# Kernel tuning notes

Measured on AMD Instinct MI355X. Metric: run time of the kernel, lower is better.

The kernel has to match this reference:

```python
import jax, jax.numpy as jnp
import numpy as np

L, N, H, SQ = 24, 16384, 128, 32
D_OP, D_ATTR, D_FILT, D_OUT = 16, 56, 74, 32
D_IN = 2 * SQ + D_OP + D_ATTR  # 136
EPS = 1e-5
SLOPE = 0.01  # LeakyReLU default


def setup_inputs() -> dict:
    key = jax.random.key(0)
    ks = jax.random.split(key, 24)
    f32 = jnp.float32
    inp = {
        'op_pad': jax.random.normal(ks[0], (L, N, D_OP), f32),
        'attr_pad': jax.random.normal(ks[1], (L, N, D_ATTR), f32),
        'filter_pad': jax.random.normal(ks[2], (L, N, D_FILT), f32),
        'output_pad': jax.random.normal(ks[3], (L, N, D_OUT), f32),
        'mapping_pad': jax.random.randint(ks[4], (L, N, 2), 0, N + 1, jnp.int32),
        'batch_size': 4096,
        # filter / output squeeze linears
        'Wf': jax.random.normal(ks[5], (SQ, D_FILT), f32) * 0.05,
        'bf': jax.random.normal(ks[6], (SQ,), f32) * 0.05,
        'Wo': jax.random.normal(ks[7], (SQ, D_OUT), f32) * 0.05,
        'bo': jax.random.normal(ks[8], (SQ,), f32) * 0.05,
        # batchnorm affine params
        'g1': jnp.ones((SQ,), f32), 'beta1': jnp.zeros((SQ,), f32),
        'g2': jnp.ones((SQ,), f32), 'beta2': jnp.zeros((SQ,), f32),
        # LSTM (PyTorch layout: gates i,f,g,o stacked)
        'Wih': jax.random.normal(ks[9], (4 * H, D_IN), f32) * 0.05,
        'Whh': jax.random.normal(ks[10], (4 * H, H), f32) * 0.05,
        'bih': jax.random.normal(ks[11], (4 * H,), f32) * 0.05,
        'bhh': jax.random.normal(ks[12], (4 * H,), f32) * 0.05,
        # final MLP head
        'W1': jax.random.normal(ks[13], (20, H), f32) * 0.05,
        'b1': jax.random.normal(ks[14], (20,), f32) * 0.05,
        'W2': jax.random.normal(ks[15], (1, 20), f32) * 0.05,
        'b2': jax.random.normal(ks[16], (1,), f32) * 0.05,
    }
    return inp


def _leaky(x):
    return jnp.where(x > 0, x, SLOPE * x)


def _bn(x, g, b):
    # BatchNorm1d in training mode: batch stats (biased var), eps=1e-5
    m = jnp.mean(x, axis=0)
    v = jnp.var(x, axis=0)
    return (x - m) * jax.lax.rsqrt(v + EPS) * g + b


def _forward(op_pad, attr_pad, filter_pad, output_pad, mapping_pad, batch_size,
             Wf, bf, Wo, bo, g1, beta1, g2, beta2, Wih, Whh, bih, bhh, W1, b1, W2, b2):
    l, n = op_pad.shape[0], op_pad.shape[1]
    # squeeze filter / output features, flattened over (L*N)
    fd = _bn(_leaky(filter_pad.reshape(l * n, -1) @ Wf.T + bf), g1, beta1).reshape(l, n, SQ)
    od = _bn(_leaky(output_pad.reshape(l * n, -1) @ Wo.T + bo), g2, beta2).reshape(l, n, SQ)
    lstm_in = jnp.concatenate([op_pad, attr_pad, fd, od], axis=2)  # [L,N,D_IN]

    def step(carry, xs):
        h, c = carry                       # [N,H] previous level states
        x, mapping = xs                    # [N,D_IN], [N,2]
        mask = (mapping != 0)[..., None]   # [N,2,1]
        idx = jnp.maximum(mapping - 1, 0)  # [N,2] gather indices
        gh = jnp.sum(jnp.where(mask, h[idx], 0.0), axis=1) * 0.5  # [N,H]
        gc = jnp.sum(jnp.where(mask, c[idx], 0.0), axis=1) * 0.5
        gates = x @ Wih.T + bih + gh @ Whh.T + bhh  # [N,4H]
        i, f, g, o = jnp.split(gates, 4, axis=1)
        c_new = jax.nn.sigmoid(f) * gc + jax.nn.sigmoid(i) * jnp.tanh(g)
        h_new = jax.nn.sigmoid(o) * jnp.tanh(c_new)
        return (h_new, c_new), None

    z = jnp.zeros((n, H), lstm_in.dtype)
    # loop goes from the deepest level (index L-1) up to 0
    (h, _), _ = jax.lax.scan(step, (z, z), (lstm_in[::-1], mapping_pad[::-1]))
    out = h[:batch_size]
    out = jax.nn.sigmoid((out @ W1.T + b1) @ W2.T + b2)  # [B,1]
    return out


def reference(op_pad, attr_pad, filter_pad, output_pad, mapping_pad, batch_size,
              Wf, bf, Wo, bo, g1, beta1, g2, beta2, Wih, Whh, bih, bhh, W1, b1, W2, b2):
    return _forward(op_pad, attr_pad, filter_pad, output_pad, mapping_pad, batch_size,
                    Wf, bf, Wo, bo, g1, beta1, g2, beta2, Wih, Whh, bih, bhh, W1, b1, W2, b2)
```

## Files before the change

kernel.cpp:

```cpp
#include <hip/hip_runtime.h>
#include <hip/hip_bf16.h>

#define LL 24
#define NN 16384
#define HH 128
#define KP 288
#define LN (LL*NN)

typedef __bf16 bf16;
typedef __attribute__((ext_vector_type(8))) __bf16 bf16x8;
typedef __attribute__((ext_vector_type(4))) __bf16 bf16x4;
typedef __attribute__((ext_vector_type(2))) __bf16 bf16x2;
typedef __attribute__((ext_vector_type(4))) float f32x4;

__device__ __forceinline__ float sigm(float x){ return 1.f/(1.f+__expf(-x)); }
__device__ __forceinline__ float tanhfast(float x){
    float e = __expf(-2.f*fabsf(x));
    float t = (1.f-e)/(1.f+e);
    return x >= 0.f ? t : -t;
}
__device__ __forceinline__ void gld16(const void* g, void* l){
    __builtin_amdgcn_global_load_lds(
        (const __attribute__((address_space(1))) void*)g,
        (__attribute__((address_space(3))) void*)l, 16, 0, 0);
}

template<int D, int DP, int NQ, int TILES>
__global__ __launch_bounds__(256) void act_kernel(
    const float* __restrict__ X, const float* __restrict__ W,
    const float* __restrict__ bias, bf16* __restrict__ act,
    float* __restrict__ sums)
{
    __shared__ float xs[192*DP];
    const int tid = threadIdx.x;
    const int cg  = tid & 7;
    const int rg  = tid >> 3;
    const int rbase = rg*6;

    float bc[4];
    #pragma unroll
    for (int c=0;c<4;++c) bc[c] = bias[cg*4+c];

    float s[4] = {0,0,0,0}, qq[4] = {0,0,0,0};

    for (int tile = blockIdx.x; tile < TILES; tile += gridDim.x) {
        __syncthreads();
        const float* Xt = X + (size_t)tile * (192*D);
        for (int i = tid; i < 192*D; i += 256) {
            int r = i / D, c = i - r*D;
            xs[r*DP + c] = Xt[i];
        }
        if constexpr (4*NQ > D) {
            constexpr int PADW = 4*NQ - D;
            for (int i = tid; i < 192*PADW; i += 256) {
                int r = i / PADW, c = i - r*PADW;
                xs[r*DP + D + c] = 0.f;
            }
        }
        __syncthreads();

        float a[6][4];
        #pragma unroll
        for (int i=0;i<6;++i)
            #pragma unroll
            for (int c=0;c<4;++c) a[i][c] = 0.f;

        #pragma unroll 2
        for (int q = 0; q < NQ; ++q) {
            float4 wv[4];
            #pragma unroll
            for (int c = 0; c < 4; ++c) {
                const float* wp = W + (cg*4 + c)*D + q*4;
                if constexpr (D % 4 == 0) {
                    wv[c] = *(const float4*)wp;
                } else {
                    if ((4*NQ > D) && (q == NQ-1)) {
                        float2 lo = *(const float2*)wp;
                        wv[c] = make_float4(lo.x, lo.y, 0.f, 0.f);
                    } else {
                        float2 lo = *(const float2*)wp;
                        float2 hi = *(const float2*)(wp+2);
                        wv[c] = make_float4(lo.x, lo.y, hi.x, hi.y);
                    }
                }
            }
            #pragma unroll
            for (int i = 0; i < 6; ++i) {
                float4 xv = *(const float4*)&xs[(rbase+i)*DP + q*4];
                #pragma unroll
                for (int c = 0; c < 4; ++c) {
                    a[i][c] = fmaf(xv.x, wv[c].x, a[i][c]);
                    a[i][c] = fmaf(xv.y, wv[c].y, a[i][c]);
                    a[i][c] = fmaf(xv.z, wv[c].z, a[i][c]);
                    a[i][c] = fmaf(xv.w, wv[c].w, a[i][c]);
                }
            }
        }

        #pragma unroll
        for (int i = 0; i < 6; ++i) {
            bf16x4 pk;
            #pragma unroll
            for (int c = 0; c < 4; ++c) {
                float v = a[i][c] + bc[c];
                v = v > 0.f ? v : 0.01f*v;
                pk[c] = (bf16)v;
                s[c] += v; qq[c] += v*v;
            }
            *(bf16x4*)&act[((size_t)tile*192 + rbase + i)*32 + cg*4] = pk;
        }
    }

    __syncthreads();
    float* red = xs;
    #pragma unroll
    for (int c=0;c<4;++c){ red[tid*8 + c*2] = s[c]; red[tid*8 + c*2 + 1] = qq[c]; }
    __syncthreads();
    if (tid < 64) {
        const int ch = tid >> 1, v = tid & 1;
        const int cgr = ch >> 2, cl = ch & 3;
        float t = 0.f;
        for (int r = 0; r < 32; ++r)
            t += red[(r*8 + cgr)*8 + cl*2 + v];
        atomicAdd(&sums[v*32 + ch], t);
    }
}

__global__ void prep_wtb(const float* __restrict__ Wih, const float* __restrict__ Whh,
                         const float* __restrict__ bih, const float* __restrict__ bhh,
                         bf16* __restrict__ Wtb, float* __restrict__ b4p)
{
    const int np = blockIdx.x;
    const int k  = threadIdx.x;
    const int gate = (np>>4)&3;
    const int j = gate*128 + (np>>6)*16 + (np&15);
    if (k < KP) {
        float v = 0.f;
        if (k < 136)      v = Wih[(long)j*136 + k];
        else if (k >= 160) v = Whh[(long)j*128 + (k-160)];
        Wtb[(long)np*KP + k] = (bf16)v;
    }
    if (k == 0) b4p[np] = bih[j] + bhh[j];
}

__global__ void prep_stats(const float* __restrict__ stats,
    const float* __restrict__ g1, const float* __restrict__ beta1,
    const float* __restrict__ g2, const float* __restrict__ beta2,
    const float* __restrict__ W1, const float* __restrict__ b1,
    const float* __restrict__ W2, const float* __restrict__ b2,
    float* __restrict__ ss, float* __restrict__ wvb)
{
    const int t = threadIdx.x;
    const float inv = 1.f/(float)LN;
    if (t < 32) {
        float mean = stats[t]*inv;
        float var  = stats[32+t]*inv - mean*mean;
        float sc = g1[t]/sqrtf(var + 1e-5f);
        ss[t] = sc; ss[32+t] = beta1[t] - mean*sc;
    } else if (t < 64) {
        int c = t - 32;
        float mean = stats[64+c]*inv;
        float var  = stats[96+c]*inv - mean*mean;
        float sc = g2[c]/sqrtf(var + 1e-5f);
        ss[64+c] = sc; ss[96+c] = beta2[c] - mean*sc;
    }
    float s = 0.f;
    for (int a=0;a<20;++a) s += W2[a]*W1[a*HH + t];
    wvb[t] = s;
    if (t == 0) {
        float sb = 0.f;
        for (int a=0;a<20;++a) sb += W2[a]*b1[a];
        wvb[128] = sb + b2[0];
    }
}

__global__ __launch_bounds__(256) void build_a(
    const float* __restrict__ op, const float* __restrict__ attr,
    const bf16* __restrict__ actf, const bf16* __restrict__ acto,
    const int* __restrict__ map, const float* __restrict__ ss,
    const bf16* __restrict__ h_prev, bf16* __restrict__ A,
    int l, int first)
{
    const int n0 = blockIdx.x * 32;
    const long lbase = (long)l * NN;
    for (int i = threadIdx.x; i < 32*36; i += 256) {
        const int r = i / 36, c = i - r*36;
        const long n = n0 + r;
        const long e = lbase + n;
        const int k0 = c*8;
        bf16x8 out;
        if (c < 9) {
            const float* src = (c < 2) ? (op + e*16 + k0) : (attr + e*56 + (k0-16));
            float4 f0 = *(const float4*)src;
            float4 f1 = *(const float4*)(src+4);
            out[0]=(bf16)f0.x; out[1]=(bf16)f0.y; out[2]=(bf16)f0.z; out[3]=(bf16)f0.w;
            out[4]=(bf16)f1.x; out[5]=(bf16)f1.y; out[6]=(bf16)f1.z; out[7]=(bf16)f1.w;
        } else if (c < 17) {
            const int ch = (c < 13) ? (k0-72) : (k0-104);
            const bf16* src = (c < 13) ? (actf + e*32 + ch) : (acto + e*32 + ch);
            const float* s = ss + ((c < 13) ? 0 : 64);
            bf16x8 v = *(const bf16x8*)src;
            #pragma unroll
            for (int j=0;j<8;++j)
                out[j] = (bf16)fmaf((float)v[j], s[ch+j], s[32+ch+j]);
        } else if (c < 20) {
            #pragma unroll
            for (int j=0;j<8;++j) out[j] = (bf16)0.f;
        } else {
            const int jj = k0 - 160;
            float g[8] = {0,0,0,0,0,0,0,0};
            if (!first) {
                int2 mp = *(const int2*)&map[e*2];
                if (mp.x) { bf16x8 v = *(const bf16x8*)&h_prev[(long)(mp.x-1)*HH + jj];
                    #pragma unroll
                    for (int j=0;j<8;++j) g[j] += (float)v[j]; }
                if (mp.y) { bf16x8 v = *(const bf16x8*)&h_prev[(long)(mp.y-1)*HH + jj];
                    #pragma unroll
                    for (int j=0;j<8;++j) g[j] += (float)v[j]; }
            }
            #pragma unroll
            for (int j=0;j<8;++j) out[j] = (bf16)(0.5f*g[j]);
        }
        *(bf16x8*)&A[n*KP + k0] = out;
    }
}

__global__ __launch_bounds__(256) void lstm_gemm(
    const bf16* __restrict__ A, const bf16* __restrict__ Wtb,
    const float* __restrict__ b4p, const int* __restrict__ map,
    const float* __restrict__ c_prev, float* __restrict__ c_next,
    bf16* __restrict__ h_next, int l, int first)
{
    __shared__ bf16 As[128*32];
    __shared__ bf16 Bs[128*32];
    const int tid  = threadIdx.x;
    const int bm   = blockIdx.x;
    const int bn   = blockIdx.y;
    const int m0   = bm*128, n0p = bn*128;
    const int lane = tid & 63, w = tid >> 6;
    const int wr   = w >> 1,  wc = w & 1;

    f32x4 acc[4][4];
    #pragma unroll
    for (int ni=0; ni<4; ++ni){
        float b = b4p[n0p + wc*64 + ni*16 + (lane&15)];
        #pragma unroll
        for (int mi=0; mi<4; ++mi) acc[mi][ni] = (f32x4){b,b,b,b};
    }

    const bf16* Ab = A   + (size_t)m0*KP;
    const bf16* Bb = Wtb + (size_t)n0p*KP;
    const int lrr = lane >> 2;
    const int qs  = lane & 3;

    for (int kk=0; kk<9; ++kk){
        __syncthreads();
        #pragma unroll
        for (int hh=0; hh<2; ++hh){
            const int lr = w*32 + hh*16 + lrr;
            const int q  = qs ^ ((lr>>1)&3);
            const size_t go = (size_t)lr*KP + kk*32 + q*8;
            gld16(Ab + go, &As[(w*32 + hh*16)*32]);
            gld16(Bb + go, &Bs[(w*32 + hh*16)*32]);
        }
        __syncthreads();
        bf16x8 af[4], bfr[4];
        #pragma unroll
        for (int t4=0; t4<4; ++t4){
            const int am = wr*64 + t4*16 + (lane&15);
            af[t4] = *(const bf16x8*)&As[am*32 + (((lane>>4) ^ ((am>>1)&3))<<3)];
            const int bn_ = wc*64 + t4*16 + (lane&15);
            bfr[t4] = *(const bf16x8*)&Bs[bn_*32 + (((lane>>4) ^ ((bn_>>1)&3))<<3)];
        }
        #pragma unroll
        for (int mi=0; mi<4; ++mi)
            #pragma unroll
            for (int ni=0; ni<4; ++ni)
                acc[mi][ni] = __builtin_amdgcn_mfma_f32_16x16x32_bf16(
                    af[mi], bfr[ni], acc[mi][ni], 0, 0, 0);
    }

    const long lbase = (long)l * NN;
    const int cell = bn*32 + wc*16 + (lane&15);
    #pragma unroll
    for (int mi=0; mi<4; ++mi){
        const int rbase = m0 + wr*64 + mi*16 + (lane>>4)*4;
        #pragma unroll
        for (int reg=0; reg<4; ++reg){
            const int n = rbase + reg;
            float gc = 0.f;
            if (!first){
                int2 mp = *(const int2*)&map[(lbase+n)*2];
                if (mp.x) gc += c_prev[(long)(mp.x-1)*HH + cell];
                if (mp.y) gc += c_prev[(long)(mp.y-1)*HH + cell];
                gc *= 0.5f;
            }
            float cn = sigm(acc[mi][1][reg])*gc
                     + sigm(acc[mi][0][reg])*tanhfast(acc[mi][2][reg]);
            float hn = sigm(acc[mi][3][reg])*tanhfast(cn);
            c_next[(long)n*HH + cell] = cn;
            h_next[(long)n*HH + cell] = (bf16)hn;
        }
    }
}

__global__ __launch_bounds__(256) void final_k(
    const bf16* __restrict__ h, const float* __restrict__ wvb,
    float* __restrict__ out, int rows)
{
    int gt = blockIdx.x*256 + threadIdx.x;
    int row = gt >> 6;
    int lane = gt & 63;
    if (row >= rows) return;
    float v = fmaf((float)h[(long)row*HH + lane], wvb[lane],
                   (float)h[(long)row*HH + 64 + lane] * wvb[64+lane]);
    #pragma unroll
    for (int off=32; off>0; off>>=1) v += __shfl_down(v, off);
    if (lane == 0) out[row] = sigm(v + wvb[128]);
}

extern "C" void kernel_launch(void* const* d_in, const int* in_sizes, int n_in,
                              void* d_out, int out_size, void* d_ws, size_t ws_size,
                              hipStream_t stream)
{
    const float* op      = (const float*)d_in[0];
    const float* attr    = (const float*)d_in[1];
    const float* filt    = (const float*)d_in[2];
    const float* outp    = (const float*)d_in[3];
    const int*   mapping = (const int*)d_in[4];
    const float* Wf  = (const float*)d_in[6];
    const float* bf_ = (const float*)d_in[7];
    const float* Wo  = (const float*)d_in[8];
    const float* bo  = (const float*)d_in[9];
    const float* g1  = (const float*)d_in[10];
    const float* be1 = (const float*)d_in[11];
    const float* g2  = (const float*)d_in[12];
    const float* be2 = (const float*)d_in[13];
    const float* Wih = (const float*)d_in[14];
    const float* Whh = (const float*)d_in[15];
    const float* bih = (const float*)d_in[16];
    const float* bhh = (const float*)d_in[17];
    const float* W1  = (const float*)d_in[18];
    const float* b1  = (const float*)d_in[19];
    const float* W2  = (const float*)d_in[20];
    const float* b2  = (const float*)d_in[21];

    char* p = (char*)d_ws;
    auto alloc = [&](size_t bytes){ char* r = p; p += (bytes + 255) & ~255ull; return r; };
    bf16* actf = (bf16*)alloc((size_t)LN*32*2);
    bf16* acto = (bf16*)alloc((size_t)LN*32*2);
    bf16* h0   = (bf16*)alloc((size_t)NN*HH*2);
    bf16* h1   = (bf16*)alloc((size_t)NN*HH*2);
    float* c0  = (float*)alloc((size_t)NN*HH*4);
    float* c1  = (float*)alloc((size_t)NN*HH*4);
    bf16* Abuf = (bf16*)alloc((size_t)NN*KP*2);
    bf16* Wtb  = (bf16*)alloc((size_t)512*KP*2);
    float* b4p = (float*)alloc(512*4);
    float* stats=(float*)alloc(128*4);
    float* ssb = (float*)alloc(128*4);
    float* wvb = (float*)alloc(132*4);

    hipMemsetAsync(stats, 0, 128*sizeof(float), stream);
    act_kernel<74, 84, 19, 2048><<<512, 256, 0, stream>>>(filt, Wf, bf_, actf, stats);
    act_kernel<32, 36,  8, 2048><<<1024, 256, 0, stream>>>(outp, Wo, bo, acto, stats+64);
    prep_wtb<<<512, 320, 0, stream>>>(Wih, Whh, bih, bhh, Wtb, b4p);
    prep_stats<<<1, 128, 0, stream>>>(stats, g1, be1, g2, be2, W1, b1, W2, b2, ssb, wvb);

    bf16*  hb[2] = {h0, h1};
    float* cb[2] = {c0, c1};
    for (int t = 0; t < LL; ++t) {
        const int l = (LL-1) - t;
        const int first = (t == 0);
        build_a<<<NN/32, 256, 0, stream>>>(op, attr, actf, acto, mapping, ssb,
                                           hb[t&1], Abuf, l, first);
        lstm_gemm<<<dim3(128,4), 256, 0, stream>>>(Abuf, Wtb, b4p, mapping,
            cb[t&1], cb[(t+1)&1], hb[(t+1)&1], l, first);
    }
    final_k<<<(out_size*64 + 255)/256, 256, 0, stream>>>(hb[0], wvb, (float*)d_out, out_size);
}
```

Measured before the change: 1.370 ms.

## Move squeeze linears onto MFMA with split-bf16 three-term precision emulation

Replaces the scalar-FMA squeeze linear kernels for the filter and output features with an MFMA kernel. Inputs and weights are each split into bf16 high and low parts, and three MFMA products are summed to approximate fp32 accuracy. Weights are pre-split by a small prep kernel and held in registers, input tiles are staged in LDS as bf16 pairs, and the batch-norm statistics are reduced through LDS atomics. The goal is to cut the ALU-bound cost of these pre-LSTM kernels. The split-precision approximation adds conversion work and LDS pressure.

```diff
diff --git a/kernel.cpp b/kernel.cpp
--- a/kernel.cpp
+++ b/kernel.cpp
@@ -25,105 +25,168 @@
         (__attribute__((address_space(3))) void*)l, 16, 0, 0);
 }
 
-template<int D, int DP, int NQ, int TILES>
-__global__ __launch_bounds__(256) void act_kernel(
-    const float* __restrict__ X, const float* __restrict__ W,
+template<int D, int KQ>
+__global__ void prep_wsplit(const float* __restrict__ W, bf16* __restrict__ Wsp)
+{
+    for (int idx = threadIdx.x; idx < KQ*256; idx += blockDim.x) {
+        const int j   = idx & 7;
+        const int col = (idx >> 3) & 31;
+        const int kq  = idx >> 8;
+        const int k   = kq*8 + j;
+        float v = (k < D) ? W[col*D + k] : 0.f;
+        bf16 h = (bf16)v;
+        Wsp[idx]          = h;
+        Wsp[KQ*256 + idx] = (bf16)(v - (float)h);
+    }
+}
+
+template<int D, int KQ, int NQK>
+__global__ __launch_bounds__(256) void act_mfma(
+    const float* __restrict__ X, const bf16* __restrict__ Wsp,
     const float* __restrict__ bias, bf16* __restrict__ act,
     float* __restrict__ sums)
 {
-    __shared__ float xs[192*DP];
-    const int tid = threadIdx.x;
-    const int cg  = tid & 7;
-    const int rg  = tid >> 3;
-    const int rbase = rg*6;
-
-    float bc[4];
-    #pragma unroll
-    for (int c=0;c<4;++c) bc[c] = bias[cg*4+c];
-
-    float s[4] = {0,0,0,0}, qq[4] = {0,0,0,0};
-
+    constexpr int KSTEPS = KQ/4;
+    constexpr int TILES  = LN/128;
+    __shared__ __align__(16) bf16 XH[KQ*130*8];
+    __shared__ __align__(16) bf16 XL[KQ*130*8];
+    __shared__ float red[64];
+    const int tid  = threadIdx.x;
+    const int lane = tid & 63, w = tid >> 6;
+    const int l15  = lane & 15, l4 = lane >> 4;
+
+    if (tid < 64) red[tid] = 0.f;
+
+    if constexpr (KQ > NQK) {
+        for (int s = tid; s < (KQ-NQK)*128; s += 256) {
+            const int kq = NQK + (s >> 7), r = s & 127;
+            bf16x8 z;
+            #pragma unroll
+            for (int j=0;j<8;++j) z[j] = (bf16)0.f;
+            *(bf16x8*)&XH[(kq*130 + r)*8] = z;
+            *(bf16x8*)&XL[(kq*130 + r)*8] = z;
+        }
+    }
+
+    bf16x8 wh[KSTEPS][2], wl[KSTEPS][2];
+    #pragma unroll
+    for (int ks=0; ks<KSTEPS; ++ks)
+        #pragma unroll
+        for (int cht=0; cht<2; ++cht) {
+            const int idx = ((ks*4 + l4)*32 + cht*16 + l15)*8;
+            wh[ks][cht] = *(const bf16x8*)&Wsp[idx];
+            wl[ks][cht] = *(const bf16x8*)&Wsp[KQ*256 + idx];
+        }
+    float4 bb[2];
+    #pragma unroll
+    for (int cht=0; cht<2; ++cht) bb[cht] = *(const float4*)&bias[cht*16 + l4*4];
+
+    float sst[2][4], ssq[2][4];
+    #pragma unroll
+    for (int c=0;c<2;++c)
+        #pragma unroll
+        for (int r=0;r<4;++r){ sst[c][r]=0.f; ssq[c][r]=0.f; }
+
+    const int rowb = w*32;
     for (int tile = blockIdx.x; tile < TILES; tile += gridDim.x) {
         __syncthreads();
-        const float* Xt = X + (size_t)tile * (192*D);
-        for (int i = tid; i < 192*D; i += 256) {
-            int r = i / D, c = i - r*D;
-            xs[r*DP + c] = Xt[i];
-        }
-        if constexpr (4*NQ > D) {
-            constexpr int PADW = 4*NQ - D;
-            for (int i = tid; i < 192*PADW; i += 256) {
-                int r = i / PADW, c = i - r*PADW;
-                xs[r*DP + D + c] = 0.f;
-            }
+        const float* Xt = X + (size_t)tile*128*D;
+        #pragma unroll
+        for (int it = 0; it < (128*NQK)/256; ++it) {
+            const int t = it*256 + tid;
+            const int r = t / NQK, q = t - r*NQK;
+            const float* src = Xt + (size_t)r*D + q*8;
+            float xv[8];
+            if constexpr (D % 8 != 0) {
+                if (q == NQK-1) {
+                    #pragma unroll
+                    for (int j=0;j<8;++j) xv[j] = (j < D-(NQK-1)*8) ? src[j] : 0.f;
+                } else {
+                    float2 p0 = *(const float2*)(src);
+                    float2 p1 = *(const float2*)(src+2);
+                    float2 p2 = *(const float2*)(src+4);
+                    float2 p3 = *(const float2*)(src+6);
+                    xv[0]=p0.x; xv[1]=p0.y; xv[2]=p1.x; xv[3]=p1.y;
+                    xv[4]=p2.x; xv[5]=p2.y; xv[6]=p3.x; xv[7]=p3.y;
+                }
+            } else {
+                float4 f0 = *(const float4*)src;
+                float4 f1 = *(const float4*)(src+4);
+                xv[0]=f0.x; xv[1]=f0.y; xv[2]=f0.z; xv[3]=f0.w;
+                xv[4]=f1.x; xv[5]=f1.y; xv[6]=f1.z; xv[7]=f1.w;
+            }
+            bf16x8 h8, l8;
+            #pragma unroll
+            for (int j=0;j<8;++j){
+                float x = xv[j];
+                bf16 hh = (bf16)x;
+                h8[j] = hh;
+                l8[j] = (bf16)(x - (float)hh);
+            }
+            const int slot = (q*130 + r)*8;
+            *(bf16x8*)&XH[slot] = h8;
+            *(bf16x8*)&XL[slot] = l8;
         }
         __syncthreads();
 
-        float a[6][4];
-        #pragma unroll
-        for (int i=0;i<6;++i)
-            #pragma unroll
-            for (int c=0;c<4;++c) a[i][c] = 0.f;
-
-        #pragma unroll 2
-        for (int q = 0; q < NQ; ++q) {
-            float4 wv[4];
-            #pragma unroll
-            for (int c = 0; c < 4; ++c) {
-                const float* wp = W + (cg*4 + c)*D + q*4;
-                if constexpr (D % 4 == 0) {
-                    wv[c] = *(const float4*)wp;
-                } else {
-                    if ((4*NQ > D) && (q == NQ-1)) {
-                        float2 lo = *(const float2*)wp;
-                        wv[c] = make_float4(lo.x, lo.y, 0.f, 0.f);
-                    } else {
-                        float2 lo = *(const float2*)wp;
-                        float2 hi = *(const float2*)(wp+2);
-                        wv[c] = make_float4(lo.x, lo.y, hi.x, hi.y);
-                    }
+        f32x4 acc[2][2];
+        #pragma unroll
+        for (int cht=0; cht<2; ++cht)
+            #pragma unroll
+            for (int rt=0; rt<2; ++rt)
+                acc[cht][rt] = (f32x4){bb[cht].x, bb[cht].y, bb[cht].z, bb[cht].w};
+
+        #pragma unroll
+        for (int ks=0; ks<KSTEPS; ++ks) {
+            bf16x8 xh[2], xl[2];
+            #pragma unroll
+            for (int rt=0; rt<2; ++rt) {
+                const int slot = ((ks*4 + l4)*130 + rowb + rt*16 + l15)*8;
+                xh[rt] = *(const bf16x8*)&XH[slot];
+                xl[rt] = *(const bf16x8*)&XL[slot];
+            }
+            #pragma unroll
+            for (int cht=0; cht<2; ++cht)
+                #pragma unroll
+                for (int rt=0; rt<2; ++rt) {
+                    acc[cht][rt] = __builtin_amdgcn_mfma_f32_16x16x32_bf16(
+                        wh[ks][cht], xh[rt], acc[cht][rt], 0,0,0);
+                    acc[cht][rt] = __builtin_amdgcn_mfma_f32_16x16x32_bf16(
+                        wl[ks][cht], xh[rt], acc[cht][rt], 0,0,0);
+                    acc[cht][rt] = __builtin_amdgcn_mfma_f32_16x16x32_bf16(
+                        wh[ks][cht], xl[rt], acc[cht][rt], 0,0,0);
                 }
-            }
-            #pragma unroll
-            for (int i = 0; i < 6; ++i) {
-                float4 xv = *(const float4*)&xs[(rbase+i)*DP + q*4];
+        }
+
+        #pragma unroll
+        for (int cht=0; cht<2; ++cht)
+            #pragma unroll
+            for (int rt=0; rt<2; ++rt) {
+                bf16x4 pk;
                 #pragma unroll
-                for (int c = 0; c < 4; ++c) {
-                    a[i][c] = fmaf(xv.x, wv[c].x, a[i][c]);
-                    a[i][c] = fmaf(xv.y, wv[c].y, a[i][c]);
-                    a[i][c] = fmaf(xv.z, wv[c].z, a[i][c]);
-                    a[i][c] = fmaf(xv.w, wv[c].w, a[i][c]);
+                for (int reg=0; reg<4; ++reg) {
+                    float u = acc[cht][rt][reg];
+                    u = u > 0.f ? u : 0.01f*u;
+                    pk[reg] = (bf16)u;
+                    sst[cht][reg] += u;
+                    ssq[cht][reg] += u*u;
                 }
-            }
-        }
-
-        #pragma unroll
-        for (int i = 0; i < 6; ++i) {
-            bf16x4 pk;
-            #pragma unroll
-            for (int c = 0; c < 4; ++c) {
-                float v = a[i][c] + bc[c];
-                v = v > 0.f ? v : 0.01f*v;
-                pk[c] = (bf16)v;
-                s[c] += v; qq[c] += v*v;
-            }
-            *(bf16x4*)&act[((size_t)tile*192 + rbase + i)*32 + cg*4] = pk;
-        }
+                const long row = (long)tile*128 + rowb + rt*16 + l15;
+                *(bf16x4*)&act[row*32 + cht*16 + l4*4] = pk;
+            }
     }
 
     __syncthreads();
-    float* red = xs;
-    #pragma unroll
-    for (int c=0;c<4;++c){ red[tid*8 + c*2] = s[c]; red[tid*8 + c*2 + 1] = qq[c]; }
+    #pragma unroll
+    for (int cht=0; cht<2; ++cht)
+        #pragma unroll
+        for (int reg=0; reg<4; ++reg) {
+            const int ch = cht*16 + l4*4 + reg;
+            atomicAdd(&red[ch],      sst[cht][reg]);
+            atomicAdd(&red[32+ch],   ssq[cht][reg]);
+        }
     __syncthreads();
-    if (tid < 64) {
-        const int ch = tid >> 1, v = tid & 1;
-        const int cgr = ch >> 2, cl = ch & 3;
-        float t = 0.f;
-        for (int r = 0; r < 32; ++r)
-            t += red[(r*8 + cgr)*8 + cl*2 + v];
-        atomicAdd(&sums[v*32 + ch], t);
-    }
+    if (tid < 64) atomicAdd(&sums[tid], red[tid]);
 }
 
 __global__ void prep_wtb(const float* __restrict__ Wih, const float* __restrict__ Whh,
@@ -359,10 +422,14 @@
     float* stats=(float*)alloc(128*4);
     float* ssb = (float*)alloc(128*4);
     float* wvb = (float*)alloc(132*4);
+    bf16* wspf = (bf16*)alloc((size_t)12*256*2*2);
+    bf16* wspo = (bf16*)alloc((size_t)4*256*2*2);
 
     hipMemsetAsync(stats, 0, 128*sizeof(float), stream);
-    act_kernel<74, 84, 19, 2048><<<512, 256, 0, stream>>>(filt, Wf, bf_, actf, stats);
-    act_kernel<32, 36,  8, 2048><<<1024, 256, 0, stream>>>(outp, Wo, bo, acto, stats+64);
+    prep_wsplit<74,12><<<1, 256, 0, stream>>>(Wf, wspf);
+    prep_wsplit<32, 4><<<1, 256, 0, stream>>>(Wo, wspo);
+    act_mfma<74,12,10><<<768, 256, 0, stream>>>(filt, wspf, bf_, actf, stats);
+    act_mfma<32, 4, 4><<<1536, 256, 0, stream>>>(outp, wspo, bo, acto, stats+64);
     prep_wtb<<<512, 320, 0, stream>>>(Wih, Whh, bih, bhh, Wtb, b4p);
     prep_stats<<<1, 128, 0, stream>>>(stats, g1, be1, g2, be2, W1, b1, W2, b2, ssb, wvb);
 
```

Result: faster. 1.321 ms (-3.5%).
